# Performance work log

Hardware: AMD Instinct MI355X
Metric: run time of the kernel (lower is better)

Reference implementation:

```python
import jax, jax.numpy as jnp
import numpy as np

TOPK_RATIO = 0.2
ALIGN_WEIGHT = 1.0
REG_WEIGHT = 0.1
EPS_LN = 1e-6
EPS_COS = 1e-8


def setup_inputs() -> dict:
    key = jax.random.key(0)
    k1, k2, k3, k4, k5 = jax.random.split(key, 5)
    B, C, H, W = 8, 256, 200, 200
    return {
        "bev_map": jax.random.normal(k1, (B, C, H, W), dtype=jnp.float32),
        "prior_warp": jax.random.normal(k2, (B, C, H, W), dtype=jnp.float32),
        "dx_m": jax.random.normal(k3, (B,), dtype=jnp.float32),
        "dy_m": jax.random.normal(k4, (B,), dtype=jnp.float32),
        "dtheta": jax.random.normal(k5, (B,), dtype=jnp.float32),
    }


def _channel_layer_norm(x):
    # per-pixel mean/std over channel dim; torch std is unbiased (ddof=1)
    mu = jnp.mean(x, axis=1, keepdims=True)
    sigma = jnp.std(x, axis=1, keepdims=True, ddof=1) + EPS_LN
    return (x - mu) / sigma


def reference(bev_map, prior_warp, dx_m, dy_m, dtheta):
    B, C, H, W = bev_map.shape
    bev_norm = _channel_layer_norm(bev_map)      # [B,C,H,W]
    prior_norm = _channel_layer_norm(prior_warp)  # [B,C,H,W]

    # squared-sum score per pixel, flattened over spatial dims
    score = jnp.sum(bev_map * bev_map, axis=1).reshape(B, H * W)  # [B,HW]
    k = max(1, int(TOPK_RATIO * H * W))
    _, idx = jax.lax.top_k(score, k)             # [B,k]

    idx_bc = jnp.broadcast_to(idx[:, None, :], (B, C, k))
    bev_topk = jnp.take_along_axis(bev_norm.reshape(B, C, H * W), idx_bc, axis=2)
    prior_topk = jnp.take_along_axis(prior_norm.reshape(B, C, H * W), idx_bc, axis=2)

    # cosine similarity over channel dim (torch eps semantics: clamp each norm)
    num = jnp.sum(bev_topk * prior_topk, axis=1)                       # [B,k]
    na = jnp.sqrt(jnp.sum(bev_topk * bev_topk, axis=1))
    nb = jnp.sqrt(jnp.sum(prior_topk * prior_topk, axis=1))
    sim = num / (jnp.maximum(na, EPS_COS) * jnp.maximum(nb, EPS_COS))
    align_loss = jnp.mean(1.0 - sim)

    reg_loss = jnp.mean(dx_m * dx_m + dy_m * dy_m) + jnp.mean(dtheta * dtheta)
    return ALIGN_WEIGHT * align_loss + REG_WEIGHT * reg_loss
```

## Files before the change

### kernel.cpp

```cpp
#include <hip/hip_runtime.h>
#include <math.h>

#define BATCH 8
#define CCH 256
#define HW 40000
#define KSEL 8000
#define EPS_LN 1e-6f
#define EPS_COS 1e-8f

#define NCOPY 16
#define HSTRIDE 257

__device__ __forceinline__ unsigned int mono_key(float x) {
  unsigned int u = __float_as_uint(x);
  return (u & 0x80000000u) ? ~u : (u | 0x80000000u);
}

__global__ __launch_bounds__(256) void pixel_stats_kernel(
    const float* __restrict__ A, const float* __restrict__ B,
    float* __restrict__ score, float* __restrict__ contrib) {
  int tid = blockIdx.x * blockDim.x + threadIdx.x;
  if (tid >= BATCH * HW) return;
  int b = tid / HW;
  int p = tid - b * HW;
  const float* a  = A + (size_t)b * CCH * HW + p;
  const float* bb = B + (size_t)b * CCH * HW + p;

  float sa = 0.f, ssa = 0.f, sb = 0.f, ssb = 0.f, dab = 0.f;
#pragma unroll 8
  for (int c = 0; c < CCH; ++c) {
    float x = a[c * HW];
    float y = bb[c * HW];
    sa  += x;     ssa += x * x;
    sb  += y;     ssb += y * y;
    dab += x * y;
  }

  score[tid] = ssa;

  const float invC = 1.0f / (float)CCH;
  float mua = sa * invC, mub = sb * invC;
  float cssa = fmaxf(ssa - (float)CCH * mua * mua, 0.f);
  float cssb = fmaxf(ssb - (float)CCH * mub * mub, 0.f);
  float cdot = dab - (float)CCH * mua * mub;

  float siga = sqrtf(cssa / (float)(CCH - 1)) + EPS_LN;
  float sigb = sqrtf(cssb / (float)(CCH - 1)) + EPS_LN;
  float num = cdot / (siga * sigb);
  float na = sqrtf(cssa) / siga;
  float nb = sqrtf(cssb) / sigb;
  float sim = num / (fmaxf(na, EPS_COS) * fmaxf(nb, EPS_COS));
  contrib[tid] = 1.0f - sim;
}

__global__ __launch_bounds__(1024) void topk_sum_kernel(
    const float* __restrict__ score, const float* __restrict__ contrib,
    float* __restrict__ batch_sums) {
  int b = blockIdx.x;
  const float* s  = score   + b * HW;
  const float* ct = contrib + b * HW;

  __shared__ unsigned int hist[NCOPY * HSTRIDE];
  __shared__ unsigned int sel_digit, sel_remaining, tie_cnt;
  __shared__ float red[1024];

  const int copy = (threadIdx.x >> 6) & (NCOPY - 1);
  unsigned int prefix = 0;
  unsigned int remaining = KSEL;

  for (int round = 0; round < 4; ++round) {
    int shift = 24 - 8 * round;
    for (int i = threadIdx.x; i < NCOPY * HSTRIDE; i += blockDim.x) hist[i] = 0;
    __syncthreads();

    for (int i = threadIdx.x; i < HW; i += blockDim.x) {
      unsigned int key = mono_key(s[i]);
      if (round == 0 || (key >> (shift + 8)) == prefix) {
        atomicAdd(&hist[copy * HSTRIDE + ((key >> shift) & 255u)], 1u);
      }
    }
    __syncthreads();

    if (threadIdx.x == 0) {
      unsigned int cum = 0;
      int d = 255;
      for (; d >= 0; --d) {
        unsigned int c = 0;
        for (int cp = 0; cp < NCOPY; ++cp) c += hist[cp * HSTRIDE + d];
        if (cum + c >= remaining) break;
        cum += c;
      }
      sel_digit = (unsigned int)d;
      sel_remaining = remaining - cum;
      tie_cnt = 0;
    }
    __syncthreads();
    prefix = (prefix << 8) | sel_digit;
    remaining = sel_remaining;
    __syncthreads();
  }

  const unsigned int T = prefix;
  float partial = 0.f;
  for (int i = threadIdx.x; i < HW; i += blockDim.x) {
    unsigned int key = mono_key(s[i]);
    if (key > T) {
      partial += ct[i];
    } else if (key == T) {
      unsigned int old = atomicAdd(&tie_cnt, 1u);
      if (old < remaining) partial += ct[i];
    }
  }

  red[threadIdx.x] = partial;
  __syncthreads();
  for (int off = 512; off > 0; off >>= 1) {
    if ((int)threadIdx.x < off) red[threadIdx.x] += red[threadIdx.x + off];
    __syncthreads();
  }
  if (threadIdx.x == 0) batch_sums[b] = red[0];
}

__global__ void finalize_kernel(const float* __restrict__ batch_sums,
                                const float* __restrict__ dx,
                                const float* __restrict__ dy,
                                const float* __restrict__ dth,
                                float* __restrict__ out) {
  if (threadIdx.x == 0 && blockIdx.x == 0) {
    float s = 0.f;
    for (int b = 0; b < BATCH; ++b) s += batch_sums[b];
    float align = s / (float)(BATCH * KSEL);
    float r1 = 0.f, r2 = 0.f;
    for (int b = 0; b < BATCH; ++b) {
      r1 += dx[b] * dx[b] + dy[b] * dy[b];
      r2 += dth[b] * dth[b];
    }
    r1 /= (float)BATCH;
    r2 /= (float)BATCH;
    out[0] = align + 0.1f * (r1 + r2);
  }
}

extern "C" void kernel_launch(void* const* d_in, const int* in_sizes, int n_in,
                              void* d_out, int out_size, void* d_ws, size_t ws_size,
                              hipStream_t stream) {
  const float* bev   = (const float*)d_in[0];
  const float* prior = (const float*)d_in[1];
  const float* dx    = (const float*)d_in[2];
  const float* dy    = (const float*)d_in[3];
  const float* dth   = (const float*)d_in[4];
  float* out = (float*)d_out;

  float* score   = (float*)d_ws;
  float* contrib = score + BATCH * HW;
  float* bsums   = contrib + BATCH * HW;

  const int total = BATCH * HW;
  pixel_stats_kernel<<<(total + 255) / 256, 256, 0, stream>>>(bev, prior, score, contrib);
  topk_sum_kernel<<<BATCH, 1024, 0, stream>>>(score, contrib, bsums);
  finalize_kernel<<<1, 64, 0, stream>>>(bsums, dx, dy, dth, out);
}
```

Measured before the change: 757.9 us.

## Split top-k selection into multi-block 16-bit radix passes and vectorize stats loads

Replaces the single-block-per-batch 4-round 8-bit radix select with two 16-bit radix histogram passes spread across 40 blocks per batch using global atomics, plus separate select kernels that find the threshold bin via a block-wide suffix scan. The final masked sum is also split across slices and combined with float atomics. The pixel statistics kernel now loads float4 so each thread handles four pixels. This targets the serialized top-k stage running on only 8 blocks, at the cost of extra kernel launches, a zeroing pass over 1M histogram words, and nondeterministic float atomic accumulation.

```diff
diff --git a/kernel.cpp b/kernel.cpp
--- a/kernel.cpp
+++ b/kernel.cpp
@@ -4,140 +4,210 @@
 #define BATCH 8
 #define CCH 256
 #define HW 40000
+#define HW4 (HW / 4)
 #define KSEL 8000
 #define EPS_LN 1e-6f
 #define EPS_COS 1e-8f
-
-#define NCOPY 16
-#define HSTRIDE 257
+#define SLICES 40
+#define SLICE_LEN (HW / SLICES)
+
+#define OFF_SCORE   0
+#define OFF_CONTRIB 320000
+#define OFF_HIST1   640000
+#define OFF_HIST2   1164288
+#define OFF_PREFIX  1688576
+#define OFF_REM1    1688584
+#define OFF_TKEY    1688592
+#define OFF_REM2    1688600
+#define OFF_TIE     1688608
+#define OFF_BSUMS   1688616
 
 __device__ __forceinline__ unsigned int mono_key(float x) {
   unsigned int u = __float_as_uint(x);
   return (u & 0x80000000u) ? ~u : (u | 0x80000000u);
+}
+
+__global__ __launch_bounds__(256) void zero_kernel(unsigned int* __restrict__ ws) {
+  const int n4 = (2 * BATCH * 65536) / 4;
+  uint4* p = (uint4*)(ws + OFF_HIST1);
+  uint4 z = {0u, 0u, 0u, 0u};
+  for (int i = blockIdx.x * blockDim.x + threadIdx.x; i < n4; i += gridDim.x * blockDim.x)
+    p[i] = z;
+  if (blockIdx.x == 0 && threadIdx.x < BATCH) ws[OFF_BSUMS + threadIdx.x] = 0u;
 }
 
 __global__ __launch_bounds__(256) void pixel_stats_kernel(
     const float* __restrict__ A, const float* __restrict__ B,
     float* __restrict__ score, float* __restrict__ contrib) {
   int tid = blockIdx.x * blockDim.x + threadIdx.x;
-  if (tid >= BATCH * HW) return;
-  int b = tid / HW;
-  int p = tid - b * HW;
-  const float* a  = A + (size_t)b * CCH * HW + p;
-  const float* bb = B + (size_t)b * CCH * HW + p;
-
-  float sa = 0.f, ssa = 0.f, sb = 0.f, ssb = 0.f, dab = 0.f;
+  if (tid >= BATCH * HW4) return;
+  int b = tid / HW4;
+  int p4 = tid - b * HW4;
+  const float4* a  = (const float4*)(A + (size_t)b * CCH * HW) + p4;
+  const float4* bb = (const float4*)(B + (size_t)b * CCH * HW) + p4;
+
+  float sa[4] = {0, 0, 0, 0}, ssa[4] = {0, 0, 0, 0};
+  float sb[4] = {0, 0, 0, 0}, ssb[4] = {0, 0, 0, 0}, dab[4] = {0, 0, 0, 0};
+#pragma unroll 4
+  for (int c = 0; c < CCH; ++c) {
+    float4 x = a[(size_t)c * HW4];
+    float4 y = bb[(size_t)c * HW4];
+    float xs[4] = {x.x, x.y, x.z, x.w};
+    float ys[4] = {y.x, y.y, y.z, y.w};
+#pragma unroll
+    for (int j = 0; j < 4; ++j) {
+      sa[j] += xs[j];
+      ssa[j] = fmaf(xs[j], xs[j], ssa[j]);
+      sb[j] += ys[j];
+      ssb[j] = fmaf(ys[j], ys[j], ssb[j]);
+      dab[j] = fmaf(xs[j], ys[j], dab[j]);
+    }
+  }
+
+  float scv[4], cov[4];
+  const float invC = 1.0f / (float)CCH;
+#pragma unroll
+  for (int j = 0; j < 4; ++j) {
+    scv[j] = ssa[j];
+    float mua = sa[j] * invC, mub = sb[j] * invC;
+    float cssa = fmaxf(ssa[j] - (float)CCH * mua * mua, 0.f);
+    float cssb = fmaxf(ssb[j] - (float)CCH * mub * mub, 0.f);
+    float cdot = dab[j] - (float)CCH * mua * mub;
+    float siga = sqrtf(cssa / (float)(CCH - 1)) + EPS_LN;
+    float sigb = sqrtf(cssb / (float)(CCH - 1)) + EPS_LN;
+    float num = cdot / (siga * sigb);
+    float na = sqrtf(cssa) / siga;
+    float nb = sqrtf(cssb) / sigb;
+    cov[j] = 1.0f - num / (fmaxf(na, EPS_COS) * fmaxf(nb, EPS_COS));
+  }
+  int out = b * HW + p4 * 4;
+  *(float4*)(score + out)   = make_float4(scv[0], scv[1], scv[2], scv[3]);
+  *(float4*)(contrib + out) = make_float4(cov[0], cov[1], cov[2], cov[3]);
+}
+
+__global__ __launch_bounds__(256) void hist1_kernel(
+    const float* __restrict__ score, unsigned int* __restrict__ ws) {
+  int b = blockIdx.x / SLICES;
+  int sl = blockIdx.x - b * SLICES;
+  const float* s = score + b * HW;
+  unsigned int* h = ws + OFF_HIST1 + (b << 16);
+  int base = sl * SLICE_LEN;
+  for (int i = base + threadIdx.x; i < base + SLICE_LEN; i += 256) {
+    unsigned int key = mono_key(s[i]);
+    atomicAdd(&h[key >> 16], 1u);
+  }
+}
+
+__global__ __launch_bounds__(256) void hist2_kernel(
+    const float* __restrict__ score, unsigned int* __restrict__ ws) {
+  int b = blockIdx.x / SLICES;
+  int sl = blockIdx.x - b * SLICES;
+  const float* s = score + b * HW;
+  unsigned int pref = ws[OFF_PREFIX + b];
+  unsigned int* h = ws + OFF_HIST2 + (b << 16);
+  int base = sl * SLICE_LEN;
+  for (int i = base + threadIdx.x; i < base + SLICE_LEN; i += 256) {
+    unsigned int key = mono_key(s[i]);
+    if ((key >> 16) == pref) atomicAdd(&h[key & 0xFFFFu], 1u);
+  }
+}
+
+__global__ __launch_bounds__(1024) void select_kernel(unsigned int* __restrict__ ws,
+                                                      int phase) {
+  int b = blockIdx.x;
+  const unsigned int* h = ws + (phase ? OFF_HIST2 : OFF_HIST1) + (b << 16);
+  unsigned int K = phase ? ws[OFF_REM1 + b] : (unsigned int)KSEL;
+
+  __shared__ unsigned int chunk[1024];
+  __shared__ unsigned int suf[1024];
+  __shared__ unsigned int s_chunk_idx, s_cum_above;
+  __shared__ unsigned int bins[64];
+
+  int t = threadIdx.x;
+  unsigned int sum = 0;
 #pragma unroll 8
-  for (int c = 0; c < CCH; ++c) {
-    float x = a[c * HW];
-    float y = bb[c * HW];
-    sa  += x;     ssa += x * x;
-    sb  += y;     ssb += y * y;
-    dab += x * y;
-  }
-
-  score[tid] = ssa;
-
-  const float invC = 1.0f / (float)CCH;
-  float mua = sa * invC, mub = sb * invC;
-  float cssa = fmaxf(ssa - (float)CCH * mua * mua, 0.f);
-  float cssb = fmaxf(ssb - (float)CCH * mub * mub, 0.f);
-  float cdot = dab - (float)CCH * mua * mub;
-
-  float siga = sqrtf(cssa / (float)(CCH - 1)) + EPS_LN;
-  float sigb = sqrtf(cssb / (float)(CCH - 1)) + EPS_LN;
-  float num = cdot / (siga * sigb);
-  float na = sqrtf(cssa) / siga;
-  float nb = sqrtf(cssb) / sigb;
-  float sim = num / (fmaxf(na, EPS_COS) * fmaxf(nb, EPS_COS));
-  contrib[tid] = 1.0f - sim;
-}
-
-__global__ __launch_bounds__(1024) void topk_sum_kernel(
+  for (int i = 0; i < 64; ++i) sum += h[t * 64 + i];
+  chunk[t] = sum;
+  suf[t] = sum;
+  __syncthreads();
+  for (int off = 1; off < 1024; off <<= 1) {
+    unsigned int v = (t + off < 1024) ? suf[t + off] : 0u;
+    __syncthreads();
+    suf[t] += v;
+    __syncthreads();
+  }
+  unsigned int above = (t == 1023) ? 0u : suf[t + 1];
+  if (suf[t] >= K && above < K) { s_chunk_idx = (unsigned int)t; s_cum_above = above; }
+  __syncthreads();
+  if (t < 64) bins[t] = h[s_chunk_idx * 64 + t];
+  __syncthreads();
+  if (t == 0) {
+    unsigned int cum = s_cum_above;
+    int d = 63;
+    for (; d >= 0; --d) {
+      if (cum + bins[d] >= K) break;
+      cum += bins[d];
+    }
+    unsigned int binidx = s_chunk_idx * 64 + (unsigned int)d;
+    if (phase == 0) {
+      ws[OFF_PREFIX + b] = binidx;
+      ws[OFF_REM1 + b] = K - cum;
+    } else {
+      ws[OFF_TKEY + b] = (ws[OFF_PREFIX + b] << 16) | binidx;
+      ws[OFF_REM2 + b] = K - cum;
+      ws[OFF_TIE + b] = 0u;
+    }
+  }
+}
+
+__global__ __launch_bounds__(256) void sum_kernel(
     const float* __restrict__ score, const float* __restrict__ contrib,
-    float* __restrict__ batch_sums) {
-  int b = blockIdx.x;
-  const float* s  = score   + b * HW;
+    unsigned int* __restrict__ ws) {
+  int b = blockIdx.x / SLICES;
+  int sl = blockIdx.x - b * SLICES;
+  const float* s = score + b * HW;
   const float* ct = contrib + b * HW;
-
-  __shared__ unsigned int hist[NCOPY * HSTRIDE];
-  __shared__ unsigned int sel_digit, sel_remaining, tie_cnt;
-  __shared__ float red[1024];
-
-  const int copy = (threadIdx.x >> 6) & (NCOPY - 1);
-  unsigned int prefix = 0;
-  unsigned int remaining = KSEL;
-
-  for (int round = 0; round < 4; ++round) {
-    int shift = 24 - 8 * round;
-    for (int i = threadIdx.x; i < NCOPY * HSTRIDE; i += blockDim.x) hist[i] = 0;
-    __syncthreads();
-
-    for (int i = threadIdx.x; i < HW; i += blockDim.x) {
-      unsigned int key = mono_key(s[i]);
-      if (round == 0 || (key >> (shift + 8)) == prefix) {
-        atomicAdd(&hist[copy * HSTRIDE + ((key >> shift) & 255u)], 1u);
-      }
-    }
-    __syncthreads();
-
-    if (threadIdx.x == 0) {
-      unsigned int cum = 0;
-      int d = 255;
-      for (; d >= 0; --d) {
-        unsigned int c = 0;
-        for (int cp = 0; cp < NCOPY; ++cp) c += hist[cp * HSTRIDE + d];
-        if (cum + c >= remaining) break;
-        cum += c;
-      }
-      sel_digit = (unsigned int)d;
-      sel_remaining = remaining - cum;
-      tie_cnt = 0;
-    }
-    __syncthreads();
-    prefix = (prefix << 8) | sel_digit;
-    remaining = sel_remaining;
-    __syncthreads();
-  }
-
-  const unsigned int T = prefix;
+  unsigned int T = ws[OFF_TKEY + b];
+  unsigned int rem2 = ws[OFF_REM2 + b];
+
   float partial = 0.f;
-  for (int i = threadIdx.x; i < HW; i += blockDim.x) {
+  int base = sl * SLICE_LEN;
+  for (int i = base + threadIdx.x; i < base + SLICE_LEN; i += 256) {
     unsigned int key = mono_key(s[i]);
     if (key > T) {
       partial += ct[i];
     } else if (key == T) {
-      unsigned int old = atomicAdd(&tie_cnt, 1u);
-      if (old < remaining) partial += ct[i];
-    }
-  }
-
+      unsigned int old = atomicAdd(&ws[OFF_TIE + b], 1u);
+      if (old < rem2) partial += ct[i];
+    }
+  }
+
+  __shared__ float red[256];
   red[threadIdx.x] = partial;
   __syncthreads();
-  for (int off = 512; off > 0; off >>= 1) {
-    if ((int)threadIdx.x < off) red[threadIdx.x] += red[threadIdx.x + off];
+  for (int off = 128; off > 0; off >>= 1) {
+    if (threadIdx.x < (unsigned)off) red[threadIdx.x] += red[threadIdx.x + off];
     __syncthreads();
   }
-  if (threadIdx.x == 0) batch_sums[b] = red[0];
-}
-
-__global__ void finalize_kernel(const float* __restrict__ batch_sums,
+  if (threadIdx.x == 0) atomicAdd((float*)(ws + OFF_BSUMS) + b, red[0]);
+}
+
+__global__ void finalize_kernel(const unsigned int* __restrict__ ws,
                                 const float* __restrict__ dx,
                                 const float* __restrict__ dy,
                                 const float* __restrict__ dth,
                                 float* __restrict__ out) {
   if (threadIdx.x == 0 && blockIdx.x == 0) {
+    const float* bsums = (const float*)(ws + OFF_BSUMS);
     float s = 0.f;
-    for (int b = 0; b < BATCH; ++b) s += batch_sums[b];
+    for (int b = 0; b < BATCH; ++b) s += bsums[b];
     float align = s / (float)(BATCH * KSEL);
     float r1 = 0.f, r2 = 0.f;
     for (int b = 0; b < BATCH; ++b) {
       r1 += dx[b] * dx[b] + dy[b] * dy[b];
       r2 += dth[b] * dth[b];
     }
-    r1 /= (float)BATCH;
-    r2 /= (float)BATCH;
-    out[0] = align + 0.1f * (r1 + r2);
+    out[0] = align + 0.1f * (r1 / (float)BATCH + r2 / (float)BATCH);
   }
 }
 
@@ -151,12 +221,16 @@
   const float* dth   = (const float*)d_in[4];
   float* out = (float*)d_out;
 
-  float* score   = (float*)d_ws;
-  float* contrib = score + BATCH * HW;
-  float* bsums   = contrib + BATCH * HW;
-
-  const int total = BATCH * HW;
-  pixel_stats_kernel<<<(total + 255) / 256, 256, 0, stream>>>(bev, prior, score, contrib);
-  topk_sum_kernel<<<BATCH, 1024, 0, stream>>>(score, contrib, bsums);
-  finalize_kernel<<<1, 64, 0, stream>>>(bsums, dx, dy, dth, out);
-}
+  unsigned int* ws = (unsigned int*)d_ws;
+  float* score   = (float*)ws + OFF_SCORE;
+  float* contrib = (float*)ws + OFF_CONTRIB;
+
+  zero_kernel<<<256, 256, 0, stream>>>(ws);
+  pixel_stats_kernel<<<(BATCH * HW4 + 255) / 256, 256, 0, stream>>>(bev, prior, score, contrib);
+  hist1_kernel<<<BATCH * SLICES, 256, 0, stream>>>(score, ws);
+  select_kernel<<<BATCH, 1024, 0, stream>>>(ws, 0);
+  hist2_kernel<<<BATCH * SLICES, 256, 0, stream>>>(score, ws);
+  select_kernel<<<BATCH, 1024, 0, stream>>>(ws, 1);
+  sum_kernel<<<BATCH * SLICES, 256, 0, stream>>>(score, contrib, ws);
+  finalize_kernel<<<1, 64, 0, stream>>>(ws, dx, dy, dth, out);
+}
```

Measured after the change: 714.8 us. 1.06x faster.
